# Kernel tuning notes

Hardware: AMD Instinct MI355X
Metric: run time of the kernel (lower is better)

The kernel has to match this reference:

```python
import jax, jax.numpy as jnp
import numpy as np

B, EMB, ARRAY = 4096, 512, 2
KW = KH = KC = 8
OC = 16                      # output_channel per branch
RED = OC * 2                 # SE hidden width
NUM_REL = 500
FC_IN = 3 * OC * KH * KW * KC  # 24576, flattened concat of 3 branches


def _make_chequer_perm():
    # Deterministic replication of MSLE.get_chequer_perm (perm=1).
    rng = np.random.RandomState(0)
    ent_perm = rng.permutation(EMB * (ARRAY - 1))
    rel_perm = rng.permutation(EMB)
    idxs, ei, ri = [], 0, 0
    for i in range(KC):
        for j in range(KH):
            for k in range(KW):
                for m in range(ARRAY):
                    if (i + j) % ARRAY == m:
                        idxs.append(int(rel_perm[ri]) + EMB * (ARRAY - 1)); ri += 1
                    else:
                        idxs.append(int(ent_perm[ei])); ei += 1
    return jnp.asarray(np.asarray(idxs, dtype=np.int32))


def setup_inputs() -> dict:
    key = jax.random.key(0)
    ks = jax.random.split(key, 12)
    n = lambda k, shape, s=0.05: jax.random.normal(k, shape, jnp.float32) * s
    f1_dim = ARRAY * OC * 1 * 1 * ARRAY        # (1,1,2) kernels
    f3_dim = ARRAY * OC * 1 * ARRAY * ARRAY    # (1,2,2) kernels
    f5_dim = ARRAY * OC * ARRAY * ARRAY * ARRAY  # (2,2,2) kernels
    z = lambda shape: jnp.zeros(shape, jnp.float32)
    o = lambda shape: jnp.ones(shape, jnp.float32)
    return {
        "concat_input": jax.random.normal(ks[0], (B, EMB * ARRAY), jnp.float32),
        "rel": jax.random.randint(ks[1], (B,), 0, NUM_REL),
        "chequer_perm": _make_chequer_perm(),
        "f1_table": n(ks[2], (NUM_REL, f1_dim)),
        "f3_table": n(ks[3], (NUM_REL, f3_dim)),
        "f5_table": n(ks[4], (NUM_REL, f5_dim)),
        "bn0_g": o((ARRAY,)), "bn0_b": z((ARRAY,)),
        "bn1_g": o((OC,)), "bn1_b": z((OC,)),
        "bn2_g": o((OC,)), "bn2_b": z((OC,)),
        "bn3_g": o((OC,)), "bn3_b": z((OC,)),
        "att_Wsq": n(ks[5], (OC, RED)), "att_bsq": z((RED,)),
        "att_W1": n(ks[6], (RED, OC)), "att_b1": z((OC,)),
        "att_W2": n(ks[7], (RED, OC)), "att_b2": z((OC,)),
        "att_W3": n(ks[8], (RED, OC)), "att_b3": z((OC,)),
        "fc_W": n(ks[9], (FC_IN, EMB), 0.01), "fc_b": z((EMB,)),
    }


def _bn(x, g, b, eps=1e-5):
    # BatchNorm3d, training-mode batch statistics over (N, D, H, W).
    m = x.mean(axis=(0, 2, 3, 4), keepdims=True)
    v = x.var(axis=(0, 2, 3, 4), keepdims=True)
    sh = (1, -1, 1, 1, 1)
    return (x - m) * jax.lax.rsqrt(v + eps) * g.reshape(sh) + b.reshape(sh)


def _per_sample_conv(x, w):
    # x: (B, Cin, D, H, W); w: (B, Cout, Cin, kd, kh, kw). 'same' padding,
    # even kernels pad the extra element at the high end (torch padding='same').
    conv1 = lambda xb, wb: jax.lax.conv_general_dilated(
        xb[None], wb, (1, 1, 1), 'SAME',
        dimension_numbers=('NCDHW', 'OIDHW', 'NCDHW'))[0]
    return jax.vmap(conv1)(x, w)


def reference(concat_input, rel, chequer_perm, f1_table, f3_table, f5_table,
              bn0_g, bn0_b, bn1_g, bn1_b, bn2_g, bn2_b, bn3_g, bn3_b,
              att_Wsq, att_bsq, att_W1, att_b1, att_W2, att_b2, att_W3, att_b3,
              fc_W, fc_b):
    b = concat_input.shape[0]
    # Chequered interleave of entity / relation embedding dims.
    x = concat_input[:, chequer_perm].reshape(b, ARRAY, KW, KH, KC)
    x = _bn(x, bn0_g, bn0_b)  # dropout = identity (eval)
    # Per-sample dynamic filters from relation embeddings.
    f1 = f1_table[rel].reshape(b, OC, ARRAY, 1, 1, ARRAY)
    f3 = f3_table[rel].reshape(b, OC, ARRAY, 1, ARRAY, ARRAY)
    f5 = f5_table[rel].reshape(b, OC, ARRAY, ARRAY, ARRAY, ARRAY)
    x1 = _bn(_per_sample_conv(x, f1), bn1_g, bn1_b)
    x3 = _bn(_per_sample_conv(x, f3), bn2_g, bn2_b)
    x5 = _bn(_per_sample_conv(x, f5), bn3_g, bn3_b)
    xs = x1 + x3 + x5
    # SE-style 3D attention: global pool -> shared squeeze -> 3 sigmoid gates.
    pooled = xs.mean(axis=(2, 3, 4))                       # (B, OC)
    zq = jax.nn.relu(pooled @ att_Wsq + att_bsq)           # (B, RED)
    gate = lambda W, bb: jax.nn.sigmoid(zq @ W + bb)[:, :, None, None, None]
    x1 = x1 * gate(att_W1, att_b1)
    x3 = x3 * gate(att_W2, att_b2)
    x5 = x5 * gate(att_W3, att_b3)
    out = jax.nn.relu(jnp.concatenate([x1, x3, x5], axis=1))
    out = out.reshape(b, -1)                               # (B, FC_IN)
    return out @ fc_W + fc_b                               # (B, EMB)
```

## Files before the change

### kernel.cpp

```cpp
#include <hip/hip_runtime.h>
#include <hip/hip_bf16.h>
#include <stdint.h>

typedef short s16x8 __attribute__((ext_vector_type(8)));
typedef short s16x4 __attribute__((ext_vector_type(4)));
typedef float f32x4 __attribute__((ext_vector_type(4)));

#define NB 4096
#define KTOT 24576
#define NOUT 512
#define NCH 48

__device__ __forceinline__ short f2bf(float f){
  union { float f; uint32_t u; } x; x.f = f;
  uint32_t r = (x.u + 0x7FFFu + ((x.u >> 16) & 1u)) >> 16;
  return (short)r;
}
__device__ __forceinline__ float bf2f(short s){
  union { uint32_t u; float f; } x; x.u = ((uint32_t)(uint16_t)s) << 16;
  return x.f;
}
__device__ __forceinline__ short f2bf_fast(float x){
  union { __hip_bfloat16 h; short s; } c; c.h = __float2bfloat16(x); return c.s;
}

#define GLOAD16(g, l) __builtin_amdgcn_global_load_lds( \
  (const __attribute__((address_space(1))) void*)(g), \
  (__attribute__((address_space(3))) void*)(l), 16, 0, 0)

__global__ __launch_bounds__(256) void k_colmap(const int* __restrict__ perm,
                                                int* __restrict__ chmap,
                                                float* __restrict__ statf){
  int q = blockIdx.x * 256 + threadIdx.x;
  if (q < 1024) chmap[perm[q]] = q >> 9;
  if (blockIdx.x == 0 && threadIdx.x < 4) statf[threadIdx.x] = 0.f;
}

__global__ __launch_bounds__(256) void k_bn0(const float* __restrict__ concat,
                                             const int* __restrict__ chmap,
                                             float* __restrict__ statf){
  int t = threadIdx.x;
  const int ch = chmap[(blockIdx.x*256 + t) & 1023];
  float s0=0,q0=0,s1=0,q1=0;
  for (int idx = blockIdx.x*256 + t; idx < NB*1024; idx += 2048*256){
    float v = concat[idx];
    if (ch){ s1 += v; q1 += v*v; } else { s0 += v; q0 += v*v; }
  }
  #pragma unroll
  for (int m=1;m<64;m<<=1){
    s0 += __shfl_xor(s0,m); q0 += __shfl_xor(q0,m);
    s1 += __shfl_xor(s1,m); q1 += __shfl_xor(q1,m);
  }
  __shared__ float lb[4][4];
  int wid = t>>6, lane = t&63;
  if (lane==0){ lb[wid][0]=s0; lb[wid][1]=q0; lb[wid][2]=s1; lb[wid][3]=q1; }
  __syncthreads();
  if (t==0){
    float a0=0,a1=0,a2=0,a3=0;
    #pragma unroll
    for (int w=0;w<4;w++){ a0+=lb[w][0]; a1+=lb[w][1]; a2+=lb[w][2]; a3+=lb[w][3]; }
    atomicAdd(&statf[0],a0); atomicAdd(&statf[1],a1);
    atomicAdd(&statf[2],a2); atomicAdd(&statf[3],a3);
  }
}

__global__ __launch_bounds__(256) void k_wcast(const float* __restrict__ fcW,
                                               short* __restrict__ wT){
  __shared__ float tile[64][65];
  int bid = blockIdx.x;
  int kb = (bid % 384) * 64;
  int nb = (bid / 384) * 64;
  int t = threadIdx.x;
  #pragma unroll
  for (int i=0;i<16;i++){
    int r = i*4 + (t>>6), c = t & 63;
    tile[r][c] = fcW[(size_t)(kb + r)*NOUT + nb + c];
  }
  __syncthreads();
  #pragma unroll
  for (int i=0;i<16;i++){
    int n = i*4 + (t>>6), k = t & 63;
    wT[(size_t)(nb + n)*KTOT + kb + k] = f2bf(tile[k][n]);
  }
}

__global__ __launch_bounds__(256) void k_conv(
    const float* __restrict__ concat, const int* __restrict__ perm,
    const int* __restrict__ rel,
    const float* __restrict__ f1t, const float* __restrict__ f3t,
    const float* __restrict__ f5t,
    const float* __restrict__ statf,
    const float* __restrict__ bn0g, const float* __restrict__ bn0b,
    short* __restrict__ raw, float* __restrict__ psum, float* __restrict__ psq)
{
  const int b = blockIdx.x;
  const int t = threadIdx.x;
  __shared__ float xn[2*9*9*9];
  __shared__ float filt[448];
  for (int i=t;i<1458;i+=256) xn[i]=0.f;
  int r = rel[b];
  for (int i=t;i<448;i+=256){
    float v;
    if (i < 64)       v = f1t[r*64 + i];
    else if (i < 192) v = f3t[r*128 + (i-64)];
    else              v = f5t[r*256 + (i-192)];
    filt[i]=v;
  }
  __syncthreads();
  const float n0inv = 1.f/(4096.f*512.f);
  float m0 = statf[0]*n0inv, e0 = statf[1]*n0inv;
  float m1 = statf[2]*n0inv, e1 = statf[3]*n0inv;
  float sc0 = bn0g[0]*rsqrtf(e0-m0*m0+1e-5f), sh0 = bn0b[0]-m0*sc0;
  float sc1 = bn0g[1]*rsqrtf(e1-m1*m1+1e-5f), sh1 = bn0b[1]-m1*sc1;
  for (int q=t;q<1024;q+=256){
    int col = perm[q];
    float v = concat[(size_t)b*1024 + col];
    int ch = q>>9, s = q & 511;
    int d = s>>6, h=(s>>3)&7, w=s&7;
    xn[ch*729 + d*81 + h*9 + w] = ch ? v*sc1+sh1 : v*sc0+sh0;
  }
  __syncthreads();

  const int wid = t>>6, lane = t&63;
  const int d = lane>>3, h = lane&7;
  float r00[9], r01[9], r10[9], r11[9], r20[9], r21[9], r30[9], r31[9];
  #pragma unroll
  for (int w9=0;w9<9;w9++){
    int base0 = d*81 + h*9 + w9;
    int base1 = d*81 + (h+1)*9 + w9;
    int base2 = (d+1)*81 + h*9 + w9;
    int base3 = (d+1)*81 + (h+1)*9 + w9;
    r00[w9]=xn[base0];      r01[w9]=xn[729+base0];
    r10[w9]=xn[base1];      r11[w9]=xn[729+base1];
    r20[w9]=xn[base2];      r21[w9]=xn[729+base2];
    r30[w9]=xn[base3];      r31[w9]=xn[729+base3];
  }
  const size_t rawbase = (size_t)b*KTOT;

  auto finish = [&](int c, const float* v){
    float s=0,q=0;
    #pragma unroll
    for (int p=0;p<8;p++){ s += v[p]; q += v[p]*v[p]; }
    #pragma unroll
    for (int m=1;m<64;m<<=1){ s += __shfl_xor(s,m); q += __shfl_xor(q,m); }
    if (lane==0){ psum[c*NB+b]=s; psq[c*NB+b]=q; }
    s16x8 pk;
    #pragma unroll
    for (int p=0;p<8;p++) pk[p] = f2bf_fast(v[p]);
    *reinterpret_cast<s16x8*>(raw + rawbase + (size_t)c*512 + lane*8) = pk;
  };

  #pragma unroll
  for (int i=0;i<4;i++){
    int oc = wid + 4*i;
    float c0=filt[oc*4+0], c1=filt[oc*4+1], c2=filt[oc*4+2], c3=filt[oc*4+3];
    float v[8];
    #pragma unroll
    for (int p=0;p<8;p++)
      v[p] = c0*r00[p]+c1*r00[p+1]+c2*r01[p]+c3*r01[p+1];
    finish(oc, v);
  }
  #pragma unroll
  for (int i=0;i<4;i++){
    int oc = wid + 4*i;
    const float* cf = &filt[64 + oc*8];
    float v[8];
    #pragma unroll
    for (int p=0;p<8;p++)
      v[p] = cf[0]*r00[p]+cf[1]*r00[p+1]+cf[2]*r10[p]+cf[3]*r10[p+1]
           + cf[4]*r01[p]+cf[5]*r01[p+1]+cf[6]*r11[p]+cf[7]*r11[p+1];
    finish(16+oc, v);
  }
  #pragma unroll
  for (int i=0;i<4;i++){
    int oc = wid + 4*i;
    const float* cf = &filt[192 + oc*16];
    float v[8];
    #pragma unroll
    for (int p=0;p<8;p++)
      v[p] = cf[0]*r00[p] +cf[1]*r00[p+1] +cf[2]*r10[p] +cf[3]*r10[p+1]
           + cf[4]*r20[p] +cf[5]*r20[p+1] +cf[6]*r30[p] +cf[7]*r30[p+1]
           + cf[8]*r01[p] +cf[9]*r01[p+1] +cf[10]*r11[p]+cf[11]*r11[p+1]
           + cf[12]*r21[p]+cf[13]*r21[p+1]+cf[14]*r31[p]+cf[15]*r31[p+1];
    finish(32+oc, v);
  }
}

__global__ __launch_bounds__(256) void k_bnstats(
    const float* __restrict__ psum, const float* __restrict__ psq,
    const float* __restrict__ bn1g, const float* __restrict__ bn1b,
    const float* __restrict__ bn2g, const float* __restrict__ bn2b,
    const float* __restrict__ bn3g, const float* __restrict__ bn3b,
    float* __restrict__ statf)
{
  int c = blockIdx.x, t = threadIdx.x;
  float s=0,q=0;
  for (int b=t;b<NB;b+=256){ s += psum[c*NB+b]; q += psq[c*NB+b]; }
  #pragma unroll
  for (int m=1;m<64;m<<=1){ s += __shfl_xor(s,m); q += __shfl_xor(q,m); }
  __shared__ float lb[4][2];
  int wid = t>>6, lane = t&63;
  if (lane==0){ lb[wid][0]=s; lb[wid][1]=q; }
  __syncthreads();
  if (t==0){
    s = lb[0][0]+lb[1][0]+lb[2][0]+lb[3][0];
    q = lb[0][1]+lb[1][1]+lb[2][1]+lb[3][1];
    float n = 4096.f*512.f;
    float mean = s/n, var = q/n - mean*mean;
    const float* g  = c<16 ? bn1g : (c<32 ? bn2g : bn3g);
    const float* bb = c<16 ? bn1b : (c<32 ? bn2b : bn3b);
    int oc = c & 15;
    float sc = g[oc]*rsqrtf(var + 1e-5f);
    statf[16+c] = sc;
    statf[64+c] = bb[oc] - mean*sc;
  }
}

__global__ __launch_bounds__(256) void k_se(
    const float* __restrict__ psum, const float* __restrict__ statf,
    const float* __restrict__ Wsq, const float* __restrict__ bsq,
    const float* __restrict__ W1, const float* __restrict__ b1,
    const float* __restrict__ W2, const float* __restrict__ b2,
    const float* __restrict__ W3, const float* __restrict__ b3,
    float* __restrict__ gates)
{
  int b = blockIdx.x*256 + threadIdx.x;
  float pooled[16];
  #pragma unroll
  for (int oc=0;oc<16;oc++){
    float p = 0.f;
    #pragma unroll
    for (int br=0;br<3;br++){
      int c = br*16 + oc;
      p += psum[c*NB+b]*(1.f/512.f)*statf[16+c] + statf[64+c];
    }
    pooled[oc] = p;
  }
  float zq[32];
  #pragma unroll
  for (int r2=0;r2<32;r2++){
    float z = bsq[r2];
    #pragma unroll
    for (int oc=0;oc<16;oc++) z += pooled[oc]*Wsq[oc*32+r2];
    zq[r2] = fmaxf(z, 0.f);
  }
  #pragma unroll
  for (int br=0;br<3;br++){
    const float* W  = br==0 ? W1 : (br==1 ? W2 : W3);
    const float* bb = br==0 ? b1 : (br==1 ? b2 : b3);
    #pragma unroll
    for (int oc=0;oc<16;oc++){
      float g = bb[oc];
      #pragma unroll
      for (int r2=0;r2<32;r2++) g += zq[r2]*W[r2*16+oc];
      gates[(size_t)(br*16+oc)*NB + b] = 1.f/(1.f + expf(-g));
    }
  }
}

__global__ __launch_bounds__(512, 2) void k_gemm(
    const short* __restrict__ raw, const short* __restrict__ wT,
    const float* __restrict__ scale, const float* __restrict__ shift,
    const float* __restrict__ gates, short* __restrict__ partials)
{
  const int t = threadIdx.x;
  const int bid = blockIdx.x;
  const int sk = bid & 7, mblk = bid >> 3;
  const int b0 = mblk*128;
  const int kb0 = sk*3072;

  __shared__ __align__(16) short Al[3][128*32];
  __shared__ __align__(16) short Wl[3][512*32];
  __shared__ float gscL[6*128], gshL[6*128];

  const int wid = t>>6, lane = t&63;
  const int wm = wid>>2, wn = wid&3;
  const int fr = lane&15, kq = lane>>4;

  for (int i=t;i<768;i+=512){
    int c = i>>7, r = i&127;
    int ch = sk*6 + c;
    float g = gates[(size_t)ch*NB + b0 + r];
    gscL[i] = scale[ch]*g;
    gshL[i] = shift[ch]*g;
  }
  __syncthreads();

  const int row_t = wid*16 + (lane>>2);
  const int gsw = ((lane&3) ^ ((lane>>2)&3))*8;
  const short* aSrc  = raw + (size_t)(b0+row_t)*KTOT + kb0 + gsw;
  const short* wSrc0 = wT + (size_t)(wid*64 +  0 + (lane>>2))*KTOT + kb0 + gsw;
  const short* wSrc1 = wT + (size_t)(wid*64 + 16 + (lane>>2))*KTOT + kb0 + gsw;
  const short* wSrc2 = wT + (size_t)(wid*64 + 32 + (lane>>2))*KTOT + kb0 + gsw;
  const short* wSrc3 = wT + (size_t)(wid*64 + 48 + (lane>>2))*KTOT + kb0 + gsw;
  const int aDst  = wid*16*32;
  const int wDst0 = (wid*64 +  0)*32;
  const int wDst1 = (wid*64 + 16)*32;
  const int wDst2 = (wid*64 + 32)*32;
  const int wDst3 = (wid*64 + 48)*32;

  const int so16 = (kq ^ (fr&3))<<4;
  int afb[4], bfb[8];
  #pragma unroll
  for (int m=0;m<4;m++) afb[m] = (wm*64 + m*16 + fr)*64 + so16;
  #pragma unroll
  for (int n=0;n<8;n++) bfb[n] = (wn*128 + n*16 + fr)*64 + so16;
  const int trb = row_t*32 + (lane&3)*8;

  f32x4 acc[4][8];
  #pragma unroll
  for (int m=0;m<4;m++)
    #pragma unroll
    for (int n=0;n<8;n++){ f32x4 z = {0.f,0.f,0.f,0.f}; acc[m][n]=z; }

  #define STAGE(c2, ko_) { \
    GLOAD16(aSrc  + (ko_), &Al[c2][aDst]); \
    GLOAD16(wSrc0 + (ko_), &Wl[c2][wDst0]); \
    GLOAD16(wSrc1 + (ko_), &Wl[c2][wDst1]); \
    GLOAD16(wSrc2 + (ko_), &Wl[c2][wDst2]); \
    GLOAD16(wSrc3 + (ko_), &Wl[c2][wDst3]); }

  #define XF(c1, sv1) { \
    int chl_ = (sv1)>>4; chl_ = chl_>5 ? 5 : chl_; \
    float sc_ = gscL[chl_*128 + row_t], sh_ = gshL[chl_*128 + row_t]; \
    short* p_ = &Al[c1][trb]; \
    s16x8 v_ = *reinterpret_cast<const s16x8*>(p_); \
    s16x8 o_; \
    _Pragma("unroll") \
    for (int j_=0;j_<8;j_++) o_[j_] = f2bf_fast(fmaxf(bf2f(v_[j_])*sc_+sh_, 0.f)); \
    *reinterpret_cast<s16x8*>(p_) = o_; }

  #define VMC5  asm volatile("s_waitcnt vmcnt(5)" ::: "memory")
  #define LGKM0 asm volatile("s_waitcnt lgkmcnt(0)" ::: "memory")
  #define BARRIER __builtin_amdgcn_s_barrier()

  #define STEP(sv, c0, c1, c2) { \
    STAGE(c2, ((sv)+2)*32); \
    s16x8 af_[4], bf_[8]; \
    _Pragma("unroll") \
    for (int m_=0;m_<4;m_++) \
      af_[m_] = *reinterpret_cast<const s16x8*>((const char*)Al[c0] + afb[m_]); \
    _Pragma("unroll") \
    for (int n_=0;n_<8;n_++) \
      bf_[n_] = *reinterpret_cast<const s16x8*>((const char*)Wl[c0] + bfb[n_]); \
    __builtin_amdgcn_s_setprio(1); \
    _Pragma("unroll") \
    for (int m_=0;m_<4;m_++) \
      _Pragma("unroll") \
      for (int n_=0;n_<8;n_++) \
        acc[m_][n_] = __builtin_amdgcn_mfma_f32_16x16x32_bf16( \
          af_[m_], bf_[n_], acc[m_][n_], 0,0,0); \
    __builtin_amdgcn_s_setprio(0); \
    VMC5; \
    BARRIER; \
    XF(c1, (sv)+1); \
    LGKM0; \
    BARRIER; }

  STAGE(0, 0);
  STAGE(1, 32);
  VMC5;
  XF(0, 0);
  LGKM0;
  BARRIER;

  for (int i3=0; i3<32; ++i3){
    const int s0 = 3*i3;
    STEP(s0+0, 0, 1, 2);
    STEP(s0+1, 1, 2, 0);
    STEP(s0+2, 2, 0, 1);
  }

  short* pb = partials + (size_t)sk*NB*NOUT;
  #pragma unroll
  for (int m=0;m<4;m++){
    #pragma unroll
    for (int j=0;j<4;j++){
      int row = b0 + wm*64 + m*16 + kq*4 + j;
      short* prow = pb + (size_t)row*NOUT + wn*128 + fr;
      #pragma unroll
      for (int n=0;n<8;n++) prow[n*16] = f2bf_fast(acc[m][n][j]);
    }
  }
  #undef STAGE
  #undef XF
  #undef VMC5
  #undef LGKM0
  #undef BARRIER
  #undef STEP
}

__global__ __launch_bounds__(256) void k_red(const short* __restrict__ partials,
                                             const float* __restrict__ fcb,
                                             float* __restrict__ out){
  int i = blockIdx.x*256 + threadIdx.x;
  int base = i*4;
  f32x4 v = *reinterpret_cast<const f32x4*>(fcb + (base & 511));
  #pragma unroll
  for (int sk=0;sk<8;sk++){
    s16x4 p = *reinterpret_cast<const s16x4*>(partials + (size_t)sk*2097152 + base);
    v[0] += bf2f(p[0]); v[1] += bf2f(p[1]);
    v[2] += bf2f(p[2]); v[3] += bf2f(p[3]);
  }
  *reinterpret_cast<f32x4*>(out + base) = v;
}

extern "C" void kernel_launch(void* const* d_in, const int* in_sizes, int n_in,
                              void* d_out, int out_size, void* d_ws, size_t ws_size,
                              hipStream_t stream) {
  const float* concat = (const float*)d_in[0];
  const int*   rel    = (const int*)  d_in[1];
  const int*   perm   = (const int*)  d_in[2];
  const float* f1t = (const float*)d_in[3];
  const float* f3t = (const float*)d_in[4];
  const float* f5t = (const float*)d_in[5];
  const float* bn0g=(const float*)d_in[6],  *bn0b=(const float*)d_in[7];
  const float* bn1g=(const float*)d_in[8],  *bn1b=(const float*)d_in[9];
  const float* bn2g=(const float*)d_in[10], *bn2b=(const float*)d_in[11];
  const float* bn3g=(const float*)d_in[12], *bn3b=(const float*)d_in[13];
  const float* Wsq=(const float*)d_in[14],  *bsq=(const float*)d_in[15];
  const float* W1=(const float*)d_in[16],   *b1=(const float*)d_in[17];
  const float* W2=(const float*)d_in[18],   *b2=(const float*)d_in[19];
  const float* W3=(const float*)d_in[20],   *b3=(const float*)d_in[21];
  const float* fcW=(const float*)d_in[22],  *fcb=(const float*)d_in[23];
  float* out = (float*)d_out;
  char* ws = (char*)d_ws;

  const size_t off_raw  = 0;
  const size_t off_wT   = 201326592;
  const size_t off_part = 226492416;
  const size_t off_psum = 260046848;
  const size_t off_psq  = 260833280;
  const size_t off_gate = 261619712;
  const size_t off_stat = 262406144;
  const size_t off_chm  = 262406656;
  const size_t need     = off_chm + 4096;
  if (ws_size < need) return;

  short* raw      = (short*)(ws + off_raw);
  short* wT       = (short*)(ws + off_wT);
  short* partials = (short*)(ws + off_part);
  float* psum     = (float*)(ws + off_psum);
  float* psq      = (float*)(ws + off_psq);
  float* gates    = (float*)(ws + off_gate);
  float* statf    = (float*)(ws + off_stat);
  int*   chmap    = (int*)  (ws + off_chm);

  k_colmap<<<4, 256, 0, stream>>>(perm, chmap, statf);
  k_bn0   <<<2048, 256, 0, stream>>>(concat, chmap, statf);
  k_wcast <<<3072, 256, 0, stream>>>(fcW, wT);
  k_conv  <<<4096, 256, 0, stream>>>(concat, perm, rel, f1t, f3t, f5t,
                                     statf, bn0g, bn0b, raw, psum, psq);
  k_bnstats<<<48, 256, 0, stream>>>(psum, psq, bn1g, bn1b, bn2g, bn2b,
                                    bn3g, bn3b, statf);
  k_se    <<<16, 256, 0, stream>>>(psum, statf, Wsq, bsq, W1, b1, W2, b2,
                                   W3, b3, gates);
  k_gemm  <<<256, 512, 0, stream>>>(raw, wT, statf+16, statf+64, gates, partials);
  k_red   <<<2048, 256, 0, stream>>>(partials, fcb, out);
}
```

Measured before the change: 447.5 us.

## Deepen activation prefetch to five LDS stages and use one barrier per k-step

Splits the staging of the activation tile from the weight tile. The activation tile now uses a 5-slot LDS ring with lookahead 4 and the weight tile keeps a 3-slot ring. The in-place BN/gate/ReLU transform of the next A slot now overlaps the MFMA step, and each iteration needs only one barrier instead of two. The LDS swizzle pattern also changes to a different XOR mapping. The aim is to hide global-load latency and cut synchronisation cost, at the price of more LDS per block, which could reduce occupancy, and a riskier race analysis around in-place transforms.

```diff
diff --git a/kernel.cpp b/kernel.cpp
--- a/kernel.cpp
+++ b/kernel.cpp
@@ -269,7 +269,7 @@
   const int b0 = mblk*128;
   const int kb0 = sk*3072;
 
-  __shared__ __align__(16) short Al[3][128*32];
+  __shared__ __align__(16) short Al[5][128*32];
   __shared__ __align__(16) short Wl[3][512*32];
   __shared__ float gscL[6*128], gshL[6*128];
 
@@ -287,25 +287,19 @@
   __syncthreads();
 
   const int row_t = wid*16 + (lane>>2);
-  const int gsw = ((lane&3) ^ ((lane>>2)&3))*8;
-  const short* aSrc  = raw + (size_t)(b0+row_t)*KTOT + kb0 + gsw;
-  const short* wSrc0 = wT + (size_t)(wid*64 +  0 + (lane>>2))*KTOT + kb0 + gsw;
-  const short* wSrc1 = wT + (size_t)(wid*64 + 16 + (lane>>2))*KTOT + kb0 + gsw;
-  const short* wSrc2 = wT + (size_t)(wid*64 + 32 + (lane>>2))*KTOT + kb0 + gsw;
-  const short* wSrc3 = wT + (size_t)(wid*64 + 48 + (lane>>2))*KTOT + kb0 + gsw;
-  const int aDst  = wid*16*32;
-  const int wDst0 = (wid*64 +  0)*32;
-  const int wDst1 = (wid*64 + 16)*32;
-  const int wDst2 = (wid*64 + 32)*32;
-  const int wDst3 = (wid*64 + 48)*32;
-
-  const int so16 = (kq ^ (fr&3))<<4;
+  const int gsw = (((lane&3) ^ ((lane>>3)&3)))*8;
+  const short* ap = raw + (size_t)(b0+row_t)*KTOT + kb0 + gsw;
+  const short* wp0 = wT + (size_t)(wid*64 +  0 + (lane>>2))*KTOT + kb0 + gsw;
+  const short* wp1 = wT + (size_t)(wid*64 + 16 + (lane>>2))*KTOT + kb0 + gsw;
+  const short* wp2 = wT + (size_t)(wid*64 + 32 + (lane>>2))*KTOT + kb0 + gsw;
+  const short* wp3 = wT + (size_t)(wid*64 + 48 + (lane>>2))*KTOT + kb0 + gsw;
+
+  const int so16 = (kq ^ ((fr>>1)&3))<<4;
   int afb[4], bfb[8];
   #pragma unroll
   for (int m=0;m<4;m++) afb[m] = (wm*64 + m*16 + fr)*64 + so16;
   #pragma unroll
   for (int n=0;n<8;n++) bfb[n] = (wn*128 + n*16 + fr)*64 + so16;
-  const int trb = row_t*32 + (lane&3)*8;
 
   f32x4 acc[4][8];
   #pragma unroll
@@ -313,62 +307,58 @@
     #pragma unroll
     for (int n=0;n<8;n++){ f32x4 z = {0.f,0.f,0.f,0.f}; acc[m][n]=z; }
 
-  #define STAGE(c2, ko_) { \
-    GLOAD16(aSrc  + (ko_), &Al[c2][aDst]); \
-    GLOAD16(wSrc0 + (ko_), &Wl[c2][wDst0]); \
-    GLOAD16(wSrc1 + (ko_), &Wl[c2][wDst1]); \
-    GLOAD16(wSrc2 + (ko_), &Wl[c2][wDst2]); \
-    GLOAD16(wSrc3 + (ko_), &Wl[c2][wDst3]); }
-
-  #define XF(c1, sv1) { \
-    int chl_ = (sv1)>>4; chl_ = chl_>5 ? 5 : chl_; \
-    float sc_ = gscL[chl_*128 + row_t], sh_ = gshL[chl_*128 + row_t]; \
-    short* p_ = &Al[c1][trb]; \
+  #define STAGE_W(sl, ko_) { \
+    GLOAD16(wp0 + (ko_), &Wl[sl][(wid*64 +  0)*32]); \
+    GLOAD16(wp1 + (ko_), &Wl[sl][(wid*64 + 16)*32]); \
+    GLOAD16(wp2 + (ko_), &Wl[sl][(wid*64 + 32)*32]); \
+    GLOAD16(wp3 + (ko_), &Wl[sl][(wid*64 + 48)*32]); }
+  #define STAGE_A(sl, ko_)  GLOAD16(ap + (ko_), &Al[sl][wid*512])
+
+  #define XF(sl, tl) { \
+    int ch_ = (tl)>>4; ch_ = ch_>5 ? 5 : ch_; \
+    float sc_ = gscL[ch_*128 + row_t], sh_ = gshL[ch_*128 + row_t]; \
+    short* p_ = &Al[sl][wid*512 + lane*8]; \
     s16x8 v_ = *reinterpret_cast<const s16x8*>(p_); \
     s16x8 o_; \
     _Pragma("unroll") \
     for (int j_=0;j_<8;j_++) o_[j_] = f2bf_fast(fmaxf(bf2f(v_[j_])*sc_+sh_, 0.f)); \
     *reinterpret_cast<s16x8*>(p_) = o_; }
 
-  #define VMC5  asm volatile("s_waitcnt vmcnt(5)" ::: "memory")
   #define LGKM0 asm volatile("s_waitcnt lgkmcnt(0)" ::: "memory")
-  #define BARRIER __builtin_amdgcn_s_barrier()
-
-  #define STEP(sv, c0, c1, c2) { \
-    STAGE(c2, ((sv)+2)*32); \
-    s16x8 af_[4], bf_[8]; \
-    _Pragma("unroll") \
-    for (int m_=0;m_<4;m_++) \
-      af_[m_] = *reinterpret_cast<const s16x8*>((const char*)Al[c0] + afb[m_]); \
-    _Pragma("unroll") \
-    for (int n_=0;n_<8;n_++) \
-      bf_[n_] = *reinterpret_cast<const s16x8*>((const char*)Wl[c0] + bfb[n_]); \
-    __builtin_amdgcn_s_setprio(1); \
-    _Pragma("unroll") \
-    for (int m_=0;m_<4;m_++) \
-      _Pragma("unroll") \
-      for (int n_=0;n_<8;n_++) \
-        acc[m_][n_] = __builtin_amdgcn_mfma_f32_16x16x32_bf16( \
-          af_[m_], bf_[n_], acc[m_][n_], 0,0,0); \
-    __builtin_amdgcn_s_setprio(0); \
-    VMC5; \
-    BARRIER; \
-    XF(c1, (sv)+1); \
-    LGKM0; \
-    BARRIER; }
-
-  STAGE(0, 0);
-  STAGE(1, 32);
-  VMC5;
+
+  STAGE_A(0, 0);  STAGE_A(1, 32);
+  STAGE_W(0, 0);  STAGE_A(2, 64);
+  STAGE_W(1, 32); STAGE_A(3, 96);
+  asm volatile("s_waitcnt vmcnt(10)" ::: "memory");
   XF(0, 0);
   LGKM0;
-  BARRIER;
-
-  for (int i3=0; i3<32; ++i3){
-    const int s0 = 3*i3;
-    STEP(s0+0, 0, 1, 2);
-    STEP(s0+1, 1, 2, 0);
-    STEP(s0+2, 2, 0, 1);
+
+  int sl_r = 0, sl_x = 1, sl_a = 4;
+  int sw_r = 0, sw_s = 2;
+  for (int s = 0; s < 96; ++s){
+    asm volatile("s_waitcnt vmcnt(6)" ::: "memory");
+    __builtin_amdgcn_s_barrier();
+    __builtin_amdgcn_sched_barrier(0);
+    STAGE_W(sw_s, (s+2)*32);
+    STAGE_A(sl_a, (s+4)*32);
+    const char* Ab = (const char*)Al[sl_r];
+    const char* Wb = (const char*)Wl[sw_r];
+    s16x8 af[4], bf[8];
+    #pragma unroll
+    for (int m=0;m<4;m++) af[m] = *reinterpret_cast<const s16x8*>(Ab + afb[m]);
+    #pragma unroll
+    for (int n=0;n<8;n++) bf[n] = *reinterpret_cast<const s16x8*>(Wb + bfb[n]);
+    __builtin_amdgcn_s_setprio(1);
+    #pragma unroll
+    for (int m=0;m<4;m++)
+      #pragma unroll
+      for (int n=0;n<8;n++)
+        acc[m][n] = __builtin_amdgcn_mfma_f32_16x16x32_bf16(af[m], bf[n], acc[m][n], 0,0,0);
+    __builtin_amdgcn_s_setprio(0);
+    XF(sl_x, s+1);
+    LGKM0;
+    sl_r = sl_x; sl_x = (sl_x==4)?0:sl_x+1; sl_a = (sl_a==4)?0:sl_a+1;
+    sw_r = (sw_r==2)?0:sw_r+1; sw_s = (sw_s==2)?0:sw_s+1;
   }
 
   short* pb = partials + (size_t)sk*NB*NOUT;
@@ -382,12 +372,10 @@
       for (int n=0;n<8;n++) prow[n*16] = f2bf_fast(acc[m][n][j]);
     }
   }
-  #undef STAGE
+  #undef STAGE_W
+  #undef STAGE_A
   #undef XF
-  #undef VMC5
   #undef LGKM0
-  #undef BARRIER
-  #undef STEP
 }
 
 __global__ __launch_bounds__(256) void k_red(const short* __restrict__ partials,
```

Result: faster. 422.2 us (-5.6%).
